# Kernel tuning notes

Measured on AMD Instinct MI355X. Metric: run time of the kernel, lower is better.

## Reference

```python
import jax, jax.numpy as jnp
import numpy as np

EMBED_DIM = 512
NUM_HEADS = 8
HEAD_DIM = EMBED_DIM // NUM_HEADS  # 64
ROT_T = 32  # head_dim * rope_fraction // 2
ROT_V = 32
ROPE_BASE = 10000.0


def _rope_cos_sin(idx, rot_dim, base=ROPE_BASE):
    # idx: (S,) int positions -> cos,sin: (S, rot_dim//2)
    half = rot_dim // 2
    inv_freq = 1.0 / (base ** (jnp.arange(half, dtype=jnp.float32) / half))
    angles = idx.astype(jnp.float32)[:, None] * inv_freq[None, :]  # (S, half)
    return jnp.cos(angles), jnp.sin(angles)


def _apply_rope(x, cos, sin):
    # x: (B,H,S,R) with R even; cos/sin: (S, R//2)
    xe = x[..., ::2]
    xo = x[..., 1::2]
    c = cos[None, None]  # (1,1,S,R//2)
    s = sin[None, None]
    oe = xe * c - xo * s
    oo = xe * s + xo * c
    # re-interleave even/odd lanes
    return jnp.stack([oe, oo], axis=-1).reshape(x.shape)


def setup_inputs() -> dict:
    key = jax.random.key(0)
    ks = jax.random.split(key, 5)
    B, S, D = 2, 4096, EMBED_DIM
    scale_w = 1.0 / np.sqrt(D)
    return {
        "x": jax.random.normal(ks[0], (B, S, D), dtype=jnp.float32),
        "Wq": jax.random.normal(ks[1], (D, D), dtype=jnp.float32) * scale_w,
        "Wk": jax.random.normal(ks[2], (D, D), dtype=jnp.float32) * scale_w,
        "Wv": jax.random.normal(ks[3], (D, D), dtype=jnp.float32) * scale_w,
        "Wo": jax.random.normal(ks[4], (D, D), dtype=jnp.float32) * scale_w,
        "T": 128,
        "V": 32,
    }


def reference(x, Wq, Wk, Wv, Wo, T, V):
    B, S, D = x.shape
    H, hd = NUM_HEADS, HEAD_DIM
    scale = hd ** -0.5

    def split_heads(y):
        return y.reshape(B, S, H, hd).transpose(0, 2, 1, 3)  # (B,H,S,hd)

    q = split_heads(x @ Wq.T)
    k = split_heads(x @ Wk.T)
    v = split_heads(x @ Wv.T)

    p = jnp.arange(S)
    t_idx = p // V
    v_idx = p % V
    cos_t, sin_t = _rope_cos_sin(t_idx, ROT_T)
    cos_v, sin_v = _rope_cos_sin(v_idx, ROT_V)

    te, ve = ROT_T, ROT_T + ROT_V
    q = jnp.concatenate([
        _apply_rope(q[..., :te], cos_t, sin_t),
        _apply_rope(q[..., te:ve], cos_v, sin_v),
        q[..., ve:],
    ], axis=-1)
    k = jnp.concatenate([
        _apply_rope(k[..., :te], cos_t, sin_t),
        _apply_rope(k[..., te:ve], cos_v, sin_v),
        k[..., ve:],
    ], axis=-1)

    attn = jnp.einsum("bhqd,bhkd->bhqk", q, k) * scale  # (B,H,S,S)
    attn = jax.nn.softmax(attn, axis=-1)
    y = jnp.einsum("bhqk,bhkd->bhqd", attn, v)
    y = y.transpose(0, 2, 1, 3).reshape(B, S, D)
    return y @ Wo.T
```

## Files before the change

### kernel.cpp

```cpp
#include <hip/hip_runtime.h>
#include <hip/hip_bf16.h>

#define SEQ 4096
#define BSZ 2
#define NH 8
#define HD 64
#define DMODEL 512

typedef __bf16 bf16_t;
typedef __bf16 bf16x8 __attribute__((ext_vector_type(8)));
typedef __bf16 bf16x4 __attribute__((ext_vector_type(4)));
typedef float f32x4 __attribute__((ext_vector_type(4)));

__device__ __forceinline__ f32x4 mfma16(bf16x8 a, bf16x8 b, f32x4 c) {
    return __builtin_amdgcn_mfma_f32_16x16x32_bf16(a, b, c, 0, 0, 0);
}

__device__ __forceinline__ bf16x8 ld8(const bf16_t* p) {
    return *reinterpret_cast<const bf16x8*>(p);
}

__device__ __forceinline__ uint32_t pack2(bf16_t a, bf16_t b) {
    union { bf16_t h[2]; uint32_t u; } x;
    x.h[0] = a; x.h[1] = b;
    return x.u;
}

__device__ __forceinline__ void gl_lds16(const bf16_t* g, bf16_t* l) {
    __builtin_amdgcn_global_load_lds(
        (const __attribute__((address_space(1))) uint32_t*)g,
        (__attribute__((address_space(3))) uint32_t*)l,
        16, 0, 0);
}

__global__ void cast_w(const float* __restrict__ wq, const float* __restrict__ wk,
                       const float* __restrict__ wv, const float* __restrict__ wo,
                       bf16_t* __restrict__ Wc, bf16_t* __restrict__ Wob) {
    int i = blockIdx.x * blockDim.x + threadIdx.x;
    int w = i >> 16, j = i & 65535;
    const float* src = (w == 0) ? wq : (w == 1) ? wk : (w == 2) ? wv : wo;
    bf16_t* dst = (w == 3) ? Wob : Wc + w * 262144;
    float4 v = reinterpret_cast<const float4*>(src)[j];
    bf16x4 o;
    o[0] = (bf16_t)v.x; o[1] = (bf16_t)v.y; o[2] = (bf16_t)v.z; o[3] = (bf16_t)v.w;
    reinterpret_cast<bf16x4*>(dst)[j] = o;
}

__global__ __launch_bounds__(256) void gemm_qkv(const float* __restrict__ A,
                                                const bf16_t* __restrict__ W,
                                                bf16_t* __restrict__ Qb,
                                                bf16_t* __restrict__ Kb,
                                                bf16_t* __restrict__ Vb,
                                                const int* __restrict__ Vpar) {
    __shared__ bf16_t As[2 * 128 * 32];
    __shared__ bf16_t Bs[2 * 128 * 32];
    const int lane = threadIdx.x & 63;
    const int wid = threadIdx.x >> 6;
    const int c = lane & 15, quad = lane >> 4;
    const int wm = wid & 1, wn = wid >> 1;
    const int m0 = blockIdx.x * 128;
    const int n0 = blockIdx.y * 128;

    f32x4 acc[4][4];
#pragma unroll
    for (int i = 0; i < 4; i++)
#pragma unroll
        for (int j = 0; j < 4; j++) acc[i][j] = f32x4{0.f, 0.f, 0.f, 0.f};

    const int lrow = lane >> 2;
    const int lch = lane & 3;
    const bf16_t* Bg = W + (size_t)(n0 + wid * 32 + lrow) * 512 + lch * 8;
    const int w0 = (wid * 32) * 32;
    const int w1 = (wid * 32 + 16) * 32;

    const float* Ag32 = A + (size_t)(m0 + wid * 32 + (lane >> 3)) * 512 + (lane & 7) * 4;
    bf16_t* Aw = As + (wid * 32 + (lane >> 3)) * 32 + (lane & 7) * 4;

    float4 ar[4];
#pragma unroll
    for (int i = 0; i < 4; i++)
        ar[i] = *reinterpret_cast<const float4*>(Ag32 + (size_t)i * 8 * 512);
    gl_lds16(Bg, Bs + w0);
    gl_lds16(Bg + 16 * 512, Bs + w1);

    for (int it = 0; it < 16; it++) {
        bf16_t* aw = Aw + (it & 1) * 4096;
#pragma unroll
        for (int i = 0; i < 4; i++) {
            bf16x4 c4;
            c4[0] = (bf16_t)ar[i].x; c4[1] = (bf16_t)ar[i].y;
            c4[2] = (bf16_t)ar[i].z; c4[3] = (bf16_t)ar[i].w;
            *reinterpret_cast<bf16x4*>(aw + i * 8 * 32) = c4;
        }

        __syncthreads();

        if (it + 1 < 16) {
            int k0 = (it + 1) * 32;
            int bo = ((it + 1) & 1) * 4096;
#pragma unroll
            for (int i = 0; i < 4; i++)
                ar[i] = *reinterpret_cast<const float4*>(Ag32 + (size_t)i * 8 * 512 + k0);
            gl_lds16(Bg + k0, Bs + bo + w0);
            gl_lds16(Bg + 16 * 512 + k0, Bs + bo + w1);
        }

        const bf16_t* Ab = As + (it & 1) * 4096;
        const bf16_t* Bb = Bs + (it & 1) * 4096;
        bf16x8 a[4], b[4];
#pragma unroll
        for (int i = 0; i < 4; i++) a[i] = ld8(&Ab[(wm * 64 + i * 16 + c) * 32 + quad * 8]);
#pragma unroll
        for (int j = 0; j < 4; j++) b[j] = ld8(&Bb[(wn * 64 + j * 16 + c) * 32 + quad * 8]);
        __builtin_amdgcn_s_setprio(1);
#pragma unroll
        for (int i = 0; i < 4; i++)
#pragma unroll
            for (int j = 0; j < 4; j++) acc[i][j] = mfma16(a[i], b[j], acc[i][j]);
        __builtin_amdgcn_s_setprio(0);
    }

    const int Vv = Vpar[0];
    const float qs = 0.1803368801111204f;
    const bool codd = (c & 1);

#pragma unroll
    for (int i = 0; i < 4; i++) {
        int mbase = m0 + wm * 64 + i * 16 + quad * 4;
#pragma unroll
        for (int j = 0; j < 4; j++) {
            int col = n0 + wn * 64 + j * 16 + c;
            int which = col >> 9;
            int h = (col >> 6) & 7;
            int d = col & 63;
            f32x4 v = acc[i][j];
            if (which < 2) {
                int fidx = (d & 31) >> 1;
                float inv = exp2f((float)fidx * -0.8304820237218407f);
                bool hi = (d >= 32);
                f32x4 part;
#pragma unroll
                for (int r = 0; r < 4; r++) part[r] = __shfl_xor(v[r], 1, 64);
#pragma unroll
                for (int r = 0; r < 4; r++) {
                    int s = (mbase + r) & 4095;
                    int tq = s / Vv;
                    int vq = s - tq * Vv;
                    float ang = (float)(hi ? vq : tq) * inv;
                    float sn = __sinf(ang), cs = __cosf(ang);
                    float xe = codd ? part[r] : v[r];
                    float xo = codd ? v[r] : part[r];
                    v[r] = codd ? (xe * sn + xo * cs) : (xe * cs - xo * sn);
                }
                if (which == 0) {
#pragma unroll
                    for (int r = 0; r < 4; r++) v[r] *= qs;
                }
            }
            bf16_t* dst = (which == 0) ? Qb : ((which == 1) ? Kb : Vb);

            float p0 = __shfl_xor(v[0], 1, 64);
            float p1 = __shfl_xor(v[1], 1, 64);
            float p2 = __shfl_xor(v[2], 1, 64);
            float p3 = __shfl_xor(v[3], 1, 64);
            uint32_t u0 = codd ? pack2((bf16_t)p2, (bf16_t)v[2])
                               : pack2((bf16_t)v[0], (bf16_t)p0);
            uint32_t u1 = codd ? pack2((bf16_t)p3, (bf16_t)v[3])
                               : pack2((bf16_t)v[1], (bf16_t)p1);
            int dcol = d & ~1;
            int m = mbase + (codd ? 2 : 0);
            {
                int b_ = m >> 12, s = m & 4095;
                *(uint32_t*)&dst[((size_t)(b_ * NH + h) * SEQ + s) * HD + dcol] = u0;
                m++;
                b_ = m >> 12; s = m & 4095;
                *(uint32_t*)&dst[((size_t)(b_ * NH + h) * SEQ + s) * HD + dcol] = u1;
            }
        }
    }
}

__global__ __launch_bounds__(256) void gemm_out(const bf16_t* __restrict__ A,
                                                const bf16_t* __restrict__ W,
                                                float* __restrict__ out) {
    __shared__ bf16_t As[2 * 128 * 32];
    __shared__ bf16_t Bs[2 * 64 * 32];
    const int t = threadIdx.x;
    const int lane = t & 63;
    const int wid = t >> 6;
    const int c = lane & 15, quad = lane >> 4;
    const int m0 = blockIdx.x * 128;
    const int n0 = blockIdx.y * 64;

    f32x4 acc[2][4];
#pragma unroll
    for (int i = 0; i < 2; i++)
#pragma unroll
        for (int j = 0; j < 4; j++) acc[i][j] = f32x4{0.f, 0.f, 0.f, 0.f};

    const int lrow = lane >> 2;
    const int lch = lane & 3;
    const bf16_t* Ag = A + (size_t)(m0 + wid * 32 + lrow) * 512 + lch * 8;
    const bf16_t* Bg = W + (size_t)(n0 + wid * 16 + lrow) * 512 + lch * 8;
    const int aw0 = (wid * 32) * 32;
    const int aw1 = (wid * 32 + 16) * 32;
    const int bw = (wid * 16) * 32;

    gl_lds16(Ag, As + aw0);
    gl_lds16(Ag + 16 * 512, As + aw1);
    gl_lds16(Bg, Bs + bw);

    for (int it = 0; it < 16; it++) {
        __syncthreads();

        if (it + 1 < 16) {
            int k0 = (it + 1) * 32;
            int ao = ((it + 1) & 1) * 4096;
            int bo = ((it + 1) & 1) * 2048;
            gl_lds16(Ag + k0, As + ao + aw0);
            gl_lds16(Ag + 16 * 512 + k0, As + ao + aw1);
            gl_lds16(Bg + k0, Bs + bo + bw);
        }

        const bf16_t* Ab = As + (it & 1) * 4096;
        const bf16_t* Bb = Bs + (it & 1) * 2048;
        bf16x8 a[2], b[4];
#pragma unroll
        for (int i = 0; i < 2; i++) a[i] = ld8(&Ab[(wid * 32 + i * 16 + c) * 32 + quad * 8]);
#pragma unroll
        for (int j = 0; j < 4; j++) b[j] = ld8(&Bb[(j * 16 + c) * 32 + quad * 8]);
        __builtin_amdgcn_s_setprio(1);
#pragma unroll
        for (int i = 0; i < 2; i++)
#pragma unroll
            for (int j = 0; j < 4; j++) acc[i][j] = mfma16(a[i], b[j], acc[i][j]);
        __builtin_amdgcn_s_setprio(0);
    }

#pragma unroll
    for (int i = 0; i < 2; i++) {
        int mbase = m0 + wid * 32 + i * 16 + quad * 4;
#pragma unroll
        for (int j = 0; j < 4; j++) {
            int col = n0 + j * 16 + c;
#pragma unroll
            for (int r = 0; r < 4; r++)
                out[(size_t)(mbase + r) * DMODEL + col] = acc[i][j][r];
        }
    }
}

__global__ __launch_bounds__(256, 2) void flash_attn(const bf16_t* __restrict__ Q,
                                                     const bf16_t* __restrict__ K,
                                                     const bf16_t* __restrict__ V,
                                                     bf16_t* __restrict__ Y) {
    __shared__ __align__(16) unsigned char smem[65536];

    const int t = threadIdx.x;
    const int lane = t & 63;
    const int c = lane & 15, quad = lane >> 4;
    const int wid = t >> 6;
    const int w = wid & 1;
    const int pr = wid >> 1;
    const int bh = blockIdx.x & 15;
    const int qx = blockIdx.x >> 4;
    const int qw = qx * 128 + w * 64;

    size_t base = (size_t)bh * SEQ * HD;
    const bf16_t* Qp = Q + base;
    const bf16_t* Vp = V + base + (size_t)pr * 2048 * HD;

    unsigned char* pairBase = smem + pr * 32768;

    const bf16_t* Kpb = K + base + (size_t)pr * 2048 * HD;
    int srcOff = w * 4096 + ((lane >> 3) * 128) +
                 (((lane & 7) ^ ((lane >> 3) & 3)) * 16);
    const bf16_t* kE = (const bf16_t*)((const unsigned char*)Kpb + srcOff);
    const bf16_t* kO = (const bf16_t*)((const unsigned char*)Kpb + (srcOff ^ 64));

    bf16x8 qf[4][2];
#pragma unroll
    for (int qt = 0; qt < 4; qt++)
#pragma unroll
        for (int ks = 0; ks < 2; ks++)
            qf[qt][ks] = ld8(Qp + (size_t)(qw + qt * 16 + c) * HD + ks * 32 + quad * 8);

    f32x4 acc[4][4];
#pragma unroll
    for (int qt = 0; qt < 4; qt++)
#pragma unroll
        for (int dt = 0; dt < 4; dt++) acc[qt][dt] = f32x4{0.f, 0.f, 0.f, 0.f};
    float lsum[4] = {0.f, 0.f, 0.f, 0.f};

    const int tp = t & 127;
    const int kva = 2 * (tp & 31);
    const int dc = 16 * (tp >> 5);

    bf16x8 vr0 = ld8(Vp + (size_t)kva * HD + dc);
    bf16x8 vr1 = ld8(Vp + (size_t)(kva + 1) * HD + dc);
    bf16x8 vr2 = ld8(Vp + (size_t)kva * HD + dc + 8);
    bf16x8 vr3 = ld8(Vp + (size_t)(kva + 1) * HD + dc + 8);
    {
        bf16_t* dst = (bf16_t*)(pairBase + w * 4096);
#pragma unroll
        for (int i = 0; i < 4; i++)
            gl_lds16(((i & 1) ? kO : kE) + i * 512, dst + i * 512);
        kE += 4096; kO += 4096;
    }

    for (int kt = 0; kt < 32; kt++) {
        uint32_t* vt = (uint32_t*)(pairBase + 16384 + (kt & 1) * 8192);

#pragma unroll
        for (int j = 0; j < 8; j++) {
            int d0 = dc + j;
            int sv0 = (d0 & 7) ^ ((d0 >> 3) & 7);
            vt[d0 * 32 + (((kva >> 3) ^ sv0) & 7) * 4 + ((kva & 6) >> 1)] = pack2(vr0[j], vr1[j]);
            int d1 = dc + 8 + j;
            int sv1 = (d1 & 7) ^ ((d1 >> 3) & 7);
            vt[d1 * 32 + (((kva >> 3) ^ sv1) & 7) * 4 + ((kva & 6) >> 1)] = pack2(vr2[j], vr3[j]);
        }

        __syncthreads();

        if (kt + 1 < 32) {
            int kv0n = (kt + 1) * 64;
            vr0 = ld8(Vp + (size_t)(kv0n + kva) * HD + dc);
            vr1 = ld8(Vp + (size_t)(kv0n + kva + 1) * HD + dc);
            vr2 = ld8(Vp + (size_t)(kv0n + kva) * HD + dc + 8);
            vr3 = ld8(Vp + (size_t)(kv0n + kva + 1) * HD + dc + 8);
            bf16_t* dst = (bf16_t*)(pairBase + ((kt + 1) & 1) * 8192 + w * 4096);
#pragma unroll
            for (int i = 0; i < 4; i++)
                gl_lds16(((i & 1) ? kO : kE) + i * 512, dst + i * 512);
            kE += 4096; kO += 4096;
        }

        const uint4* kl = (const uint4*)(pairBase + (kt & 1) * 8192);

        f32x4 st[4][4];
        __builtin_amdgcn_s_setprio(1);
#pragma unroll
        for (int n = 0; n < 4; n++) {
            int kvr = (n >> 1) * 32 + ((c >> 2) * 8) + ((n & 1) * 4) + (c & 3);
            int sk = (kvr & 3) | (((kvr >> 3) & 1) << 2);
            bf16x8 k0 = *reinterpret_cast<const bf16x8*>(&kl[kvr * 8 + (quad ^ sk)]);
            bf16x8 k1 = *reinterpret_cast<const bf16x8*>(&kl[kvr * 8 + ((4 + quad) ^ sk)]);
#pragma unroll
            for (int qt = 0; qt < 4; qt++) {
                f32x4 z = f32x4{0.f, 0.f, 0.f, 0.f};
                z = mfma16(k0, qf[qt][0], z);
                z = mfma16(k1, qf[qt][1], z);
                st[qt][n] = z;
            }
        }
        __builtin_amdgcn_s_setprio(0);

        bf16x8 pf[4][2];
#pragma unroll
        for (int qt = 0; qt < 4; qt++) {
            float e[4][4];
            float ls = 0.f;
#pragma unroll
            for (int n = 0; n < 4; n++)
#pragma unroll
                for (int r = 0; r < 4; r++) {
                    float v = __builtin_amdgcn_exp2f(st[qt][n][r]);
                    e[n][r] = v;
                    ls += v;
                }
            lsum[qt] += ls;
            bf16x8 f0, f1;
#pragma unroll
            for (int j = 0; j < 8; j++) {
                f0[j] = (bf16_t)e[(j >> 2)][j & 3];
                f1[j] = (bf16_t)e[2 + (j >> 2)][j & 3];
            }
            pf[qt][0] = f0;
            pf[qt][1] = f1;
        }

        __builtin_amdgcn_s_setprio(1);
#pragma unroll
        for (int dt = 0; dt < 4; dt++) {
            int d = dt * 16 + c;
            int sv = (d & 7) ^ ((d >> 3) & 7);
            bf16x8 v0f = *reinterpret_cast<const bf16x8*>(&vt[d * 32 + ((quad ^ sv) & 7) * 4]);
            bf16x8 v1f = *reinterpret_cast<const bf16x8*>(&vt[d * 32 + (((4 + quad) ^ sv) & 7) * 4]);
#pragma unroll
            for (int qt = 0; qt < 4; qt++) {
                acc[qt][dt] = mfma16(v0f, pf[qt][0], acc[qt][dt]);
                acc[qt][dt] = mfma16(v1f, pf[qt][1], acc[qt][dt]);
            }
        }
        __builtin_amdgcn_s_setprio(0);
    }

    float lred[4];
#pragma unroll
    for (int qt = 0; qt < 4; qt++) {
        float lt = lsum[qt];
        lt += __shfl_xor(lt, 16, 64);
        lt += __shfl_xor(lt, 32, 64);
        lred[qt] = lt;
    }

    __syncthreads();
    float* Ox = (float*)smem;
    float* Lx = (float*)(smem + 128 * 68 * 4);

    if (pr == 1) {
#pragma unroll
        for (int qt = 0; qt < 4; qt++) {
            int ql = w * 64 + qt * 16 + c;
#pragma unroll
            for (int dt = 0; dt < 4; dt++)
                *reinterpret_cast<f32x4*>(&Ox[ql * 68 + dt * 16 + quad * 4]) = acc[qt][dt];
            if (quad == 0) Lx[ql] = lred[qt];
        }
    }
    __syncthreads();
    if (pr == 0) {
        int b_ = bh >> 3, h = bh & 7;
#pragma unroll
        for (int qt = 0; qt < 4; qt++) {
            int ql = w * 64 + qt * 16 + c;
            float inv_l = 1.0f / (lred[qt] + Lx[ql]);
            int srow = qw + qt * 16 + c;
            bf16_t* yrow = Y + (size_t)(b_ * SEQ + srow) * DMODEL + h * HD;
#pragma unroll
            for (int dt = 0; dt < 4; dt++) {
                f32x4 o4 = acc[qt][dt] + *reinterpret_cast<const f32x4*>(&Ox[ql * 68 + dt * 16 + quad * 4]);
                bf16x4 o;
#pragma unroll
                for (int r = 0; r < 4; r++) o[r] = (bf16_t)(o4[r] * inv_l);
                *reinterpret_cast<bf16x4*>(yrow + dt * 16 + quad * 4) = o;
            }
        }
    }
}

extern "C" void kernel_launch(void* const* d_in, const int* in_sizes, int n_in,
                              void* d_out, int out_size, void* d_ws, size_t ws_size,
                              hipStream_t stream) {
    (void)in_sizes; (void)n_in; (void)out_size; (void)ws_size;
    const float* x  = (const float*)d_in[0];
    const float* Wq = (const float*)d_in[1];
    const float* Wk = (const float*)d_in[2];
    const float* Wv = (const float*)d_in[3];
    const float* Wo = (const float*)d_in[4];
    const int*   Vp = (const int*)d_in[6];
    float* out = (float*)d_out;

    bf16_t* ws  = (bf16_t*)d_ws;
    bf16_t* Wc  = ws;
    bf16_t* Wob = Wc  + 786432;
    bf16_t* Qb  = Wob + 262144;
    bf16_t* Kb  = Qb  + 4194304;
    bf16_t* Vb  = Kb  + 4194304;
    bf16_t* Yb  = Vb  + 4194304;

    cast_w<<<1024, 256, 0, stream>>>(Wq, Wk, Wv, Wo, Wc, Wob);

    gemm_qkv<<<dim3(64, 12), 256, 0, stream>>>(x, Wc, Qb, Kb, Vb, Vp);

    flash_attn<<<512, 256, 0, stream>>>(Qb, Kb, Vb, Yb);

    gemm_out<<<dim3(64, 8), 256, 0, stream>>>(Yb, Wob, out);
}
```

Measured before the change: 196.5 us.

## Compute softmax row sums with MFMA against ones and use shift for power-of-two V

The attention kernel no longer accumulates the softmax denominator with scalar float adds and cross-lane shuffles. It now multiplies a vector of bf16 ones by the bf16 probability fragments with extra MFMAs, so the sum comes from the matrix unit and matches the rounded P used for PV. In the QKV projection epilogue, integer division and modulo by V become shift and mask when V is a power of two. The change trades VALU work for 8 extra MFMAs per KV tile and 16 more accumulator registers, which could raise register pressure.

```diff
diff --git a/kernel.cpp b/kernel.cpp
--- a/kernel.cpp
+++ b/kernel.cpp
@@ -121,6 +121,8 @@
     }
 
     const int Vv = Vpar[0];
+    const bool vp2 = (Vv & (Vv - 1)) == 0;
+    const int vsh = 31 - __clz(Vv);
     const float qs = 0.1803368801111204f;
     const bool codd = (c & 1);
 
@@ -141,12 +143,25 @@
                 f32x4 part;
 #pragma unroll
                 for (int r = 0; r < 4; r++) part[r] = __shfl_xor(v[r], 1, 64);
+                int tqv[4], vqv[4];
+                if (vp2) {
+#pragma unroll
+                    for (int r = 0; r < 4; r++) {
+                        int s = (mbase + r) & 4095;
+                        tqv[r] = s >> vsh;
+                        vqv[r] = s & (Vv - 1);
+                    }
+                } else {
+#pragma unroll
+                    for (int r = 0; r < 4; r++) {
+                        int s = (mbase + r) & 4095;
+                        tqv[r] = s / Vv;
+                        vqv[r] = s - tqv[r] * Vv;
+                    }
+                }
 #pragma unroll
                 for (int r = 0; r < 4; r++) {
-                    int s = (mbase + r) & 4095;
-                    int tq = s / Vv;
-                    int vq = s - tq * Vv;
-                    float ang = (float)(hi ? vq : tq) * inv;
+                    float ang = (float)(hi ? vqv[r] : tqv[r]) * inv;
                     float sn = __sinf(ang), cs = __cosf(ang);
                     float xe = codd ? part[r] : v[r];
                     float xo = codd ? v[r] : part[r];
@@ -290,7 +305,12 @@
     for (int qt = 0; qt < 4; qt++)
 #pragma unroll
         for (int dt = 0; dt < 4; dt++) acc[qt][dt] = f32x4{0.f, 0.f, 0.f, 0.f};
-    float lsum[4] = {0.f, 0.f, 0.f, 0.f};
+    f32x4 accl[4];
+#pragma unroll
+    for (int qt = 0; qt < 4; qt++) accl[qt] = f32x4{0.f, 0.f, 0.f, 0.f};
+    bf16x8 onesv;
+#pragma unroll
+    for (int j = 0; j < 8; j++) onesv[j] = (bf16_t)1.0f;
 
     const int tp = t & 127;
     const int kva = 2 * (tp & 31);
@@ -359,22 +379,11 @@
         bf16x8 pf[4][2];
 #pragma unroll
         for (int qt = 0; qt < 4; qt++) {
-            float e[4][4];
-            float ls = 0.f;
-#pragma unroll
-            for (int n = 0; n < 4; n++)
-#pragma unroll
-                for (int r = 0; r < 4; r++) {
-                    float v = __builtin_amdgcn_exp2f(st[qt][n][r]);
-                    e[n][r] = v;
-                    ls += v;
-                }
-            lsum[qt] += ls;
             bf16x8 f0, f1;
 #pragma unroll
             for (int j = 0; j < 8; j++) {
-                f0[j] = (bf16_t)e[(j >> 2)][j & 3];
-                f1[j] = (bf16_t)e[2 + (j >> 2)][j & 3];
+                f0[j] = (bf16_t)__builtin_amdgcn_exp2f(st[qt][(j >> 2)][j & 3]);
+                f1[j] = (bf16_t)__builtin_amdgcn_exp2f(st[qt][2 + (j >> 2)][j & 3]);
             }
             pf[qt][0] = f0;
             pf[qt][1] = f1;
@@ -393,17 +402,17 @@
                 acc[qt][dt] = mfma16(v1f, pf[qt][1], acc[qt][dt]);
             }
         }
+#pragma unroll
+        for (int qt = 0; qt < 4; qt++) {
+            accl[qt] = mfma16(onesv, pf[qt][0], accl[qt]);
+            accl[qt] = mfma16(onesv, pf[qt][1], accl[qt]);
+        }
         __builtin_amdgcn_s_setprio(0);
     }
 
     float lred[4];
 #pragma unroll
-    for (int qt = 0; qt < 4; qt++) {
-        float lt = lsum[qt];
-        lt += __shfl_xor(lt, 16, 64);
-        lt += __shfl_xor(lt, 32, 64);
-        lred[qt] = lt;
-    }
+    for (int qt = 0; qt < 4; qt++) lred[qt] = accl[qt][0];
 
     __syncthreads();
     float* Ox = (float*)smem;
```

New measurement: 199.5 us. Within noise of the previous version (+1.5%).
